# Performance work log

Hardware: AMD Instinct MI355X
Metric: run time of the kernel (lower is better)

Reference implementation:

```python
import jax, jax.numpy as jnp
import numpy as np
from jax import lax

DIM = 96
B, H, W = 4, 256, 256


def setup_inputs() -> dict:
    key = jax.random.key(0)
    ks = jax.random.split(key, 20)
    f = lambda k, s, scale=0.05: (jax.random.normal(k, s, dtype=jnp.float32) * scale)
    d = DIM
    return {
        "x": jax.random.normal(ks[0], (B, d, H, W), dtype=jnp.float32),
        "prompt": jax.random.normal(ks[1], (B, d), dtype=jnp.float32),
        "scale_weights": jax.random.uniform(ks[2], (B, 3), dtype=jnp.float32),
        "ln_w": jnp.ones((d,), jnp.float32),
        "ln_b": jnp.zeros((d,), jnp.float32),
        "e0_pw_w": f(ks[3], (d, d)),       # expert0 pointwise 1x1: [out, in]
        "e0_pw_b": f(ks[4], (d,)),
        "e0_dw_w": f(ks[5], (d, 1, 3, 3)),  # depthwise 3x3
        "e0_dw_b": f(ks[6], (d,)),
        "e1_dw_w": f(ks[7], (d, 1, 3, 3)),  # depthwise 3x3, dilation 2
        "e1_dw_b": f(ks[8], (d,)),
        "e2_dw_w": f(ks[9], (d, 1, 5, 5)),  # depthwise 5x5, dilation 3
        "e2_dw_b": f(ks[10], (d,)),
        "proj_w": f(ks[11], (d, d)),
        "proj_b": f(ks[12], (d,)),
        "ffn1_w": f(ks[13], (2 * d, d)),
        "ffn1_b": f(ks[14], (2 * d,)),
        "ffn2_w": f(ks[15], (d, 2 * d)),
        "ffn2_b": f(ks[16], (d,)),
    }


def _conv1x1(x, w, b):
    # x: [B,C,H,W], w: [O,C]
    return jnp.einsum('bchw,oc->bohw', x, w) + b[None, :, None, None]


def _dwconv(x, w, b, dilation, pad):
    # depthwise conv, w: [C,1,k,k]
    c = x.shape[1]
    y = lax.conv_general_dilated(
        x, w, window_strides=(1, 1),
        padding=[(pad, pad), (pad, pad)],
        rhs_dilation=(dilation, dilation),
        feature_group_count=c,
        dimension_numbers=('NCHW', 'OIHW', 'NCHW'))
    return y + b[None, :, None, None]


def _layernorm_c(x, w, b, eps=1e-6):
    # LayerNorm over channel dim of NCHW (torch permutes to NHWC, norms last dim)
    mu = jnp.mean(x, axis=1, keepdims=True)
    var = jnp.mean((x - mu) ** 2, axis=1, keepdims=True)
    xn = (x - mu) * lax.rsqrt(var + eps)
    return xn * w[None, :, None, None] + b[None, :, None, None]


def reference(x, prompt, scale_weights, ln_w, ln_b,
              e0_pw_w, e0_pw_b, e0_dw_w, e0_dw_b,
              e1_dw_w, e1_dw_b, e2_dw_w, e2_dw_b,
              proj_w, proj_b, ffn1_w, ffn1_b, ffn2_w, ffn2_b):
    shortcut = x
    xn = _layernorm_c(x, ln_w, ln_b)

    # Three receptive-field experts (all run densely, soft-weighted)
    e0 = _dwconv(_conv1x1(xn, e0_pw_w, e0_pw_b), e0_dw_w, e0_dw_b, dilation=1, pad=1)
    e1 = _dwconv(xn, e1_dw_w, e1_dw_b, dilation=2, pad=2)
    e2 = _dwconv(xn, e2_dw_w, e2_dw_b, dilation=3, pad=6)

    w = scale_weights  # [B,3]
    x_adaptive = (w[:, 0, None, None, None] * e0
                  + w[:, 1, None, None, None] * e1
                  + w[:, 2, None, None, None] * e2)
    x_adaptive = x_adaptive * (1.0 + prompt[:, :, None, None])

    x1 = shortcut + _conv1x1(x_adaptive, proj_w, proj_b)
    h = jax.nn.gelu(_conv1x1(x1, ffn1_w, ffn1_b), approximate=False)
    out = x1 + _conv1x1(h, ffn2_w, ffn2_b)
    return out
```

## Files before the change

### kernel.cpp

```cpp
#include <hip/hip_runtime.h>
#include <hip/hip_bf16.h>

typedef __hip_bfloat16 bf16;
typedef __attribute__((ext_vector_type(8))) __bf16 bf16x8;
typedef __attribute__((ext_vector_type(4))) float  f32x4;

#define HW   65536
#define WID  256
#define CC   96
#define NB   4
static const size_t S_ELEMS = (size_t)NB * CC * HW;

__device__ __forceinline__ float lo2f(unsigned u) { unsigned x = u << 16;        return __builtin_bit_cast(float, x); }
__device__ __forceinline__ float hi2f(unsigned u) { unsigned x = u & 0xffff0000u; return __builtin_bit_cast(float, x); }
__device__ __forceinline__ unsigned short f2bu(float f) {
    return __builtin_bit_cast(unsigned short, __float2bfloat16(f));
}

__device__ __forceinline__ float gelu_erf(float v) {
    float z  = fabsf(v) * 0.70710678118654752f;
    float t  = __builtin_amdgcn_rcpf(1.f + 0.3275911f * z);
    float poly = t * (0.254829592f + t * (-0.284496736f + t * (1.421413741f
               + t * (-1.453152027f + t * 1.061405429f))));
    float erfz = 1.f - poly * __expf(-z * z);
    float erfv = copysignf(erfz, v);
    return 0.5f * v * (1.f + erfv);
}

__global__ __launch_bounds__(256) void ln_kernel(
    const float* __restrict__ x, const float* __restrict__ lw,
    const float* __restrict__ lb, bf16* __restrict__ y)
{
    int t  = blockIdx.x * 256 + threadIdx.x;
    int b  = t >> 15;
    int hw = (t & 32767) * 2;
    size_t base = (size_t)b * CC * HW + hw;

    float s0 = 0.f, s1 = 0.f, q0 = 0.f, q1 = 0.f;
    for (int c = 0; c < CC; ++c) {
        float2 v = *reinterpret_cast<const float2*>(&x[base + (size_t)c * HW]);
        s0 += v.x; s1 += v.y; q0 += v.x * v.x; q1 += v.y * v.y;
    }
    float mu0 = s0 * (1.f / 96.f), mu1 = s1 * (1.f / 96.f);
    float rs0 = rsqrtf(q0 * (1.f / 96.f) - mu0 * mu0 + 1e-6f);
    float rs1 = rsqrtf(q1 * (1.f / 96.f) - mu1 * mu1 + 1e-6f);

    for (int c = 0; c < CC; ++c) {
        float2 v = *reinterpret_cast<const float2*>(&x[base + (size_t)c * HW]);
        float g = lw[c], be = lb[c];
        bf16 o[2];
        o[0] = __float2bfloat16((v.x - mu0) * rs0 * g + be);
        o[1] = __float2bfloat16((v.y - mu1) * rs1 * g + be);
        *reinterpret_cast<uint*>(&y[base + (size_t)c * HW]) = *reinterpret_cast<uint*>(o);
    }
}

__device__ __forceinline__ int swzo(int row, int col, int width) {
    return (row * width + col) ^ ((((row & 7) ^ ((row >> 3) & 7)) << 3));
}

template <typename TI, typename TOT, int CIN, int COUT, bool GELU, bool HASRES>
__global__ __launch_bounds__(256) void conv1x1_mfma(
    const TI* __restrict__ in, const float* __restrict__ wgt,
    const float* __restrict__ bias, const float* __restrict__ resid,
    TOT* __restrict__ out)
{
    constexpr int MT     = COUT / 16;
    constexpr int KSPLIT = CIN / 96;
    constexpr int CS     = 96;
    static_assert(CIN == KSPLIT * CS, "CIN must be 96 or 192");

    __shared__ unsigned short s_w[COUT * CIN];
    __shared__ unsigned short s_x[128 * CS];
    __shared__ float          s_b[COUT];

    const int tid  = threadIdx.x;
    const int lane = tid & 63;
    const int wave = tid >> 6;
    const int q    = lane >> 4;
    const int n    = lane & 15;

    const int pos0 = blockIdx.x * 128;
    const int b    = pos0 >> 16;
    const int hw0  = pos0 & 65535;

    constexpr int C4 = CIN / 4;
    for (int k = tid; k < COUT * C4; k += 256) {
        int o = k / C4, c4 = (k - o * C4) * 4;
        float4 w4 = *reinterpret_cast<const float4*>(&wgt[o * CIN + c4]);
        ushort4 pk = make_ushort4(f2bu(w4.x), f2bu(w4.y), f2bu(w4.z), f2bu(w4.w));
        *reinterpret_cast<ushort4*>(&s_w[swzo(o, c4, CIN)]) = pk;
    }
    for (int k = tid; k < COUT; k += 256) s_b[k] = bias[k];

    const TI* inb = in + (size_t)b * CIN * HW;

    f32x4 acc[MT][2];
#pragma unroll
    for (int mt = 0; mt < MT; ++mt) {
        acc[mt][0] = {0.f, 0.f, 0.f, 0.f};
        acc[mt][1] = {0.f, 0.f, 0.f, 0.f};
    }

    const int pl0 = wave * 32 + n;
    const int pl1 = pl0 + 16;

#pragma unroll
    for (int ks = 0; ks < KSPLIT; ++ks) {
        if (ks) __syncthreads();

        for (int idx = tid; idx < CS * 16; idx += 256) {
            const int c    = idx >> 4;
            const int pblk = idx & 15;
            const int row0 = pblk * 8;
            const TI* gp = inb + (size_t)(ks * CS + c) * HW + hw0 + row0;
            alignas(16) unsigned short u[8];
            if constexpr (__is_same(TI, float)) {
                float4 a  = *reinterpret_cast<const float4*>(gp);
                float4 b2 = *reinterpret_cast<const float4*>(gp + 4);
                u[0] = f2bu(a.x);  u[1] = f2bu(a.y);  u[2] = f2bu(a.z);  u[3] = f2bu(a.w);
                u[4] = f2bu(b2.x); u[5] = f2bu(b2.y); u[6] = f2bu(b2.z); u[7] = f2bu(b2.w);
            } else {
                *reinterpret_cast<uint4*>(u) = *reinterpret_cast<const uint4*>(gp);
            }
#pragma unroll
            for (int i = 0; i < 8; ++i)
                s_x[swzo(row0 + i, c, CS)] = u[i];
        }
        __syncthreads();

#pragma unroll
        for (int kt = 0; kt < CS / 32; ++kt) {
            const int col = kt * 32 + q * 8;
            union { unsigned short u[8]; bf16x8 v; } bf0, bf1;
            *reinterpret_cast<uint4*>(bf0.u) =
                *reinterpret_cast<const uint4*>(&s_x[swzo(pl0, col, CS)]);
            *reinterpret_cast<uint4*>(bf1.u) =
                *reinterpret_cast<const uint4*>(&s_x[swzo(pl1, col, CS)]);
#pragma unroll
            for (int mt = 0; mt < MT; ++mt) {
                union { unsigned short u[8]; bf16x8 v; } fa;
                *reinterpret_cast<uint4*>(fa.u) =
                    *reinterpret_cast<const uint4*>(&s_w[swzo(mt * 16 + n, ks * CS + col, CIN)]);
                acc[mt][0] = __builtin_amdgcn_mfma_f32_16x16x32_bf16(fa.v, bf0.v, acc[mt][0], 0, 0, 0);
                acc[mt][1] = __builtin_amdgcn_mfma_f32_16x16x32_bf16(fa.v, bf1.v, acc[mt][1], 0, 0, 0);
            }
        }
    }

    const int p0 = hw0 + pl0;
    const int p1 = hw0 + pl1;
    const size_t obase = (size_t)b * COUT * HW;
#pragma unroll
    for (int mt = 0; mt < MT; ++mt) {
#pragma unroll
        for (int nt = 0; nt < 2; ++nt) {
            const int p = (nt == 0) ? p0 : p1;
#pragma unroll
            for (int r = 0; r < 4; ++r) {
                const int o = mt * 16 + q * 4 + r;
                float v = acc[mt][nt][r] + s_b[o];
                if constexpr (GELU) v = gelu_erf(v);
                const size_t idx = obase + (size_t)o * HW + p;
                if constexpr (HASRES) v += resid[idx];
                if constexpr (__is_same(TOT, float)) out[idx] = v;
                else                                 out[idx] = __float2bfloat16(v);
            }
        }
    }
}

#define XR     20
#define XPITCH 22
#define TPITCH 10
#define XCOLS  268
#define TCOLS  258

__global__ __launch_bounds__(256) void experts_kernel(
    const bf16* __restrict__ xn, const bf16* __restrict__ t0,
    const float* __restrict__ w0, const float* __restrict__ b0,
    const float* __restrict__ w1, const float* __restrict__ b1,
    const float* __restrict__ w2, const float* __restrict__ b2,
    const float* __restrict__ sw, const float* __restrict__ prompt,
    bf16* __restrict__ xa)
{
    __shared__ alignas(16) unsigned short sxT[XCOLS * XPITCH];
    __shared__ alignas(16) unsigned short stT[TCOLS * TPITCH];

    const int tid  = threadIdx.x;
    const int lane = tid & 63;
    const int wave = tid >> 6;
    const int bid = blockIdx.x;
    const int h0  = (bid & 31) * 8;
    const int bc  = bid >> 5;
    const int b   = bc / 96;
    const int c   = bc - b * 96;
    const size_t pbase = (size_t)bc * HW;

    const bf16* xp = xn + pbase;
    const bf16* tp = t0 + pbase;
    uint* sx32 = reinterpret_cast<uint*>(sxT);
    uint* st32 = reinterpret_cast<uint*>(stT);

    if (tid < 132) {
        int cc = tid / 11, d = tid - cc * 11;
        int col = (cc < 6) ? cc : 256 + cc;
        sx32[col * 11 + d] = 0u;
    } else if (tid < 142) {
        int i = tid - 132;
        int col = (i < 5) ? 0 : 257;
        int d   = (i < 5) ? i : i - 5;
        st32[col * 5 + d] = 0u;
    }

    {
        const int rp = (lane >> 2) & 7;
        const int ch = 8 * wave + (lane & 3) + ((lane >> 5) << 2);
        const int gh0 = h0 - 6 + 2 * rp, gh1 = gh0 + 1;
        union { uint4 q; unsigned short u[8]; } a, bb;
        a.q  = ((unsigned)gh0 < 256u) ? *reinterpret_cast<const uint4*>(xp + gh0 * WID + ch * 8)
                                      : make_uint4(0u, 0u, 0u, 0u);
        bb.q = ((unsigned)gh1 < 256u) ? *reinterpret_cast<const uint4*>(xp + gh1 * WID + ch * 8)
                                      : make_uint4(0u, 0u, 0u, 0u);
        const int base = 11 * (6 + 8 * ch) + rp;
#pragma unroll
        for (int j = 0; j < 8; ++j)
            sx32[base + 11 * j] = (uint)a.u[j] | ((uint)bb.u[j] << 16);
    }
    if (wave == 2) {
        const int rp = 8 + ((lane >> 2) & 1);
        const int ch = (lane & 3) + (((lane >> 3) & 7) << 2);
        const int gh0 = h0 - 6 + 2 * rp, gh1 = gh0 + 1;
        union { uint4 q; unsigned short u[8]; } a, bb;
        a.q  = ((unsigned)gh0 < 256u) ? *reinterpret_cast<const uint4*>(xp + gh0 * WID + ch * 8)
                                      : make_uint4(0u, 0u, 0u, 0u);
        bb.q = ((unsigned)gh1 < 256u) ? *reinterpret_cast<const uint4*>(xp + gh1 * WID + ch * 8)
                                      : make_uint4(0u, 0u, 0u, 0u);
        const int base = 11 * (6 + 8 * ch) + rp;
#pragma unroll
        for (int j = 0; j < 8; ++j)
            sx32[base + 11 * j] = (uint)a.u[j] | ((uint)bb.u[j] << 16);
    }
    if (wave < 2) {
        const int rp = (lane >> 3) & 3;
        const int ch = 16 * wave + (lane & 7) + ((lane >> 5) << 3);
        const int gh0 = h0 - 1 + 2 * rp, gh1 = gh0 + 1;
        union { uint4 q; unsigned short u[8]; } a, bb;
        a.q  = ((unsigned)gh0 < 256u) ? *reinterpret_cast<const uint4*>(tp + gh0 * WID + ch * 8)
                                      : make_uint4(0u, 0u, 0u, 0u);
        bb.q = ((unsigned)gh1 < 256u) ? *reinterpret_cast<const uint4*>(tp + gh1 * WID + ch * 8)
                                      : make_uint4(0u, 0u, 0u, 0u);
        const int base = 5 * (1 + 8 * ch) + rp;
#pragma unroll
        for (int j = 0; j < 8; ++j)
            st32[base + 5 * j] = (uint)a.u[j] | ((uint)bb.u[j] << 16);
    }
    if (wave == 3 && lane < 32) {
        const int rp = 4;
        const int ch = lane;
        const int gh0 = h0 - 1 + 2 * rp, gh1 = gh0 + 1;
        union { uint4 q; unsigned short u[8]; } a, bb;
        a.q  = ((unsigned)gh0 < 256u) ? *reinterpret_cast<const uint4*>(tp + gh0 * WID + ch * 8)
                                      : make_uint4(0u, 0u, 0u, 0u);
        bb.q = ((unsigned)gh1 < 256u) ? *reinterpret_cast<const uint4*>(tp + gh1 * WID + ch * 8)
                                      : make_uint4(0u, 0u, 0u, 0u);
        const int base = 5 * (1 + 8 * ch) + rp;
#pragma unroll
        for (int j = 0; j < 8; ++j)
            st32[base + 5 * j] = (uint)a.u[j] | ((uint)bb.u[j] << 16);
    }

    float wk0[9], wk1[9], wk2[25];
#pragma unroll
    for (int i = 0; i < 9; ++i)  wk0[i] = w0[c * 9 + i];
#pragma unroll
    for (int i = 0; i < 9; ++i)  wk1[i] = w1[c * 9 + i];
#pragma unroll
    for (int i = 0; i < 25; ++i) wk2[i] = w2[c * 25 + i];
    const float bb0 = b0[c], bb1 = b1[c], bb2 = b2[c];
    const float s0 = sw[b * 3 + 0], s1 = sw[b * 3 + 1], s2 = sw[b * 3 + 2];
    const float pr = 1.f + prompt[b * 96 + c];

    __syncthreads();

    const int w = tid;
    float acc0[8], acc1[8], acc2[8];
#pragma unroll
    for (int r = 0; r < 8; ++r) { acc0[r] = bb0; acc1[r] = bb1; acc2[r] = bb2; }

    const unsigned short* bx = &sxT[w * XPITCH];
    const unsigned short* bt = &stT[w * TPITCH];

#pragma unroll
    for (int kw = 0; kw < 5; ++kw) {
        float cv[20];
#pragma unroll
        for (int j = 0; j < 10; ++j) {
            unsigned u = *reinterpret_cast<const unsigned*>(&bx[kw * 3 * XPITCH + 2 * j]);
            cv[2 * j]     = lo2f(u);
            cv[2 * j + 1] = hi2f(u);
        }
#pragma unroll
        for (int kh = 0; kh < 5; ++kh) {
            const float wv = wk2[kh * 5 + kw];
#pragma unroll
            for (int r = 0; r < 8; ++r) acc2[r] += wv * cv[r + 3 * kh];
        }
        if (kw == 2) {
#pragma unroll
            for (int kh = 0; kh < 3; ++kh) {
                const float wv = wk1[kh * 3 + 1];
#pragma unroll
                for (int r = 0; r < 8; ++r) acc1[r] += wv * cv[r + 2 * kh + 4];
            }
        }
    }
#pragma unroll
    for (int kwh = 0; kwh < 2; ++kwh) {
        const int kw = kwh * 2;
        float cv[12];
#pragma unroll
        for (int j = 0; j < 6; ++j) {
            unsigned u = *reinterpret_cast<const unsigned*>(&bx[(4 + 2 * kw) * XPITCH + 4 + 2 * j]);
            cv[2 * j]     = lo2f(u);
            cv[2 * j + 1] = hi2f(u);
        }
#pragma unroll
        for (int kh = 0; kh < 3; ++kh) {
            const float wv = wk1[kh * 3 + kw];
#pragma unroll
            for (int r = 0; r < 8; ++r) acc1[r] += wv * cv[r + 2 * kh];
        }
    }
#pragma unroll
    for (int kw = 0; kw < 3; ++kw) {
        float cv[10];
#pragma unroll
        for (int j = 0; j < 5; ++j) {
            unsigned u = *reinterpret_cast<const unsigned*>(&bt[kw * TPITCH + 2 * j]);
            cv[2 * j]     = lo2f(u);
            cv[2 * j + 1] = hi2f(u);
        }
#pragma unroll
        for (int kh = 0; kh < 3; ++kh) {
            const float wv = wk0[kh * 3 + kw];
#pragma unroll
            for (int r = 0; r < 8; ++r) acc0[r] += wv * cv[r + kh];
        }
    }

    bf16* op = xa + pbase + (size_t)h0 * WID + w;
#pragma unroll
    for (int r = 0; r < 8; ++r) {
        float v = (s0 * acc0[r] + s1 * acc1[r] + s2 * acc2[r]) * pr;
        op[r * WID] = __float2bfloat16(v);
    }
}

extern "C" void kernel_launch(void* const* d_in, const int* in_sizes, int n_in,
                              void* d_out, int out_size, void* d_ws, size_t ws_size,
                              hipStream_t stream)
{
    const float* x       = (const float*)d_in[0];
    const float* prompt  = (const float*)d_in[1];
    const float* sw      = (const float*)d_in[2];
    const float* ln_w    = (const float*)d_in[3];
    const float* ln_b    = (const float*)d_in[4];
    const float* e0_pw_w = (const float*)d_in[5];
    const float* e0_pw_b = (const float*)d_in[6];
    const float* e0_dw_w = (const float*)d_in[7];
    const float* e0_dw_b = (const float*)d_in[8];
    const float* e1_dw_w = (const float*)d_in[9];
    const float* e1_dw_b = (const float*)d_in[10];
    const float* e2_dw_w = (const float*)d_in[11];
    const float* e2_dw_b = (const float*)d_in[12];
    const float* proj_w  = (const float*)d_in[13];
    const float* proj_b  = (const float*)d_in[14];
    const float* ffn1_w  = (const float*)d_in[15];
    const float* ffn1_b  = (const float*)d_in[16];
    const float* ffn2_w  = (const float*)d_in[17];
    const float* ffn2_b  = (const float*)d_in[18];

    float* out = (float*)d_out;
    bf16*  ws  = (bf16*)d_ws;
    bf16*  A   = ws;
    bf16*  Bt  = ws + S_ELEMS;
    bf16*  Cx  = ws + 2 * S_ELEMS;
    bf16*  E   = ws;

    ln_kernel<<<512, 256, 0, stream>>>(x, ln_w, ln_b, A);
    conv1x1_mfma<bf16, bf16, 96, 96, false, false>
        <<<2048, 256, 0, stream>>>(A, e0_pw_w, e0_pw_b, nullptr, Bt);
    experts_kernel<<<12288, 256, 0, stream>>>(A, Bt, e0_dw_w, e0_dw_b, e1_dw_w, e1_dw_b,
                                              e2_dw_w, e2_dw_b, sw, prompt, Cx);
    conv1x1_mfma<bf16, float, 96, 96, false, true>
        <<<2048, 256, 0, stream>>>(Cx, proj_w, proj_b, x, out);
    conv1x1_mfma<float, bf16, 96, 192, true, false>
        <<<2048, 256, 0, stream>>>(out, ffn1_w, ffn1_b, nullptr, E);
    conv1x1_mfma<bf16, float, 192, 96, false, true>
        <<<2048, 256, 0, stream>>>(E, ffn2_w, ffn2_b, out, out);
}
```

Measured before the change: 499.0 us.

## Make conv1x1 persistent over four tiles with register-prefetched input staging

Each conv1x1 block now loops over four 128-position tiles, loading the weights into LDS once per block rather than once per tile, and the grid shrinks to 512 blocks. Input for the next K-slice or tile is prefetched into registers while the MFMAs run on the current LDS tile, then written to LDS as packed channel pairs. This targets the repeated weight conversion and the exposed global-load latency, at the cost of more registers (launch bounds now ask for 2 blocks per SM), fewer blocks in flight, and an extra barrier per tile.

```diff
diff --git a/kernel.cpp b/kernel.cpp
--- a/kernel.cpp
+++ b/kernel.cpp
@@ -59,8 +59,11 @@
     return (row * width + col) ^ ((((row & 7) ^ ((row >> 3) & 7)) << 3));
 }
 
+#define CONV_TILES 4
+#define CONV_GRID  512
+
 template <typename TI, typename TOT, int CIN, int COUT, bool GELU, bool HASRES>
-__global__ __launch_bounds__(256) void conv1x1_mfma(
+__global__ __launch_bounds__(256, 2) void conv1x1_mfma(
     const TI* __restrict__ in, const float* __restrict__ wgt,
     const float* __restrict__ bias, const float* __restrict__ resid,
     TOT* __restrict__ out)
@@ -80,10 +83,6 @@
     const int q    = lane >> 4;
     const int n    = lane & 15;
 
-    const int pos0 = blockIdx.x * 128;
-    const int b    = pos0 >> 16;
-    const int hw0  = pos0 & 65535;
-
     constexpr int C4 = CIN / 4;
     for (int k = tid; k < COUT * C4; k += 256) {
         int o = k / C4, c4 = (k - o * C4) * 4;
@@ -93,78 +92,120 @@
     }
     for (int k = tid; k < COUT; k += 256) s_b[k] = bias[k];
 
-    const TI* inb = in + (size_t)b * CIN * HW;
-
-    f32x4 acc[MT][2];
-#pragma unroll
-    for (int mt = 0; mt < MT; ++mt) {
-        acc[mt][0] = {0.f, 0.f, 0.f, 0.f};
-        acc[mt][1] = {0.f, 0.f, 0.f, 0.f};
-    }
+    uint4  pfa[3], pfb[3];
+    float4 qa0[3], qa1[3], qb0[3], qb1[3];
+
+    auto issue_pf = [&](int tg, int ks) {
+        const int pos0 = tg * 128;
+        const int bb   = pos0 >> 16;
+        const int hw0  = pos0 & 65535;
+        const TI* inb  = in + (size_t)bb * CIN * HW;
+#pragma unroll
+        for (int k = 0; k < 3; ++k) {
+            const int idx = tid + k * 256;
+            const int cp = idx >> 4, pb = idx & 15;
+            const TI* gp = inb + (size_t)(ks * CS + 2 * cp) * HW + hw0 + pb * 8;
+            if constexpr (__is_same(TI, float)) {
+                qa0[k] = *reinterpret_cast<const float4*>(gp);
+                qa1[k] = *reinterpret_cast<const float4*>(gp + 4);
+                qb0[k] = *reinterpret_cast<const float4*>(gp + HW);
+                qb1[k] = *reinterpret_cast<const float4*>(gp + HW + 4);
+            } else {
+                pfa[k] = *reinterpret_cast<const uint4*>(gp);
+                pfb[k] = *reinterpret_cast<const uint4*>(gp + HW);
+            }
+        }
+    };
+    auto write_pf = [&]() {
+#pragma unroll
+        for (int k = 0; k < 3; ++k) {
+            const int idx = tid + k * 256;
+            const int cp = idx >> 4, pb = idx & 15;
+            unsigned short ua[8], ub[8];
+            if constexpr (__is_same(TI, float)) {
+                float fa[8] = {qa0[k].x, qa0[k].y, qa0[k].z, qa0[k].w,
+                               qa1[k].x, qa1[k].y, qa1[k].z, qa1[k].w};
+                float fb[8] = {qb0[k].x, qb0[k].y, qb0[k].z, qb0[k].w,
+                               qb1[k].x, qb1[k].y, qb1[k].z, qb1[k].w};
+#pragma unroll
+                for (int i = 0; i < 8; ++i) { ua[i] = f2bu(fa[i]); ub[i] = f2bu(fb[i]); }
+            } else {
+                *reinterpret_cast<uint4*>(ua) = pfa[k];
+                *reinterpret_cast<uint4*>(ub) = pfb[k];
+            }
+#pragma unroll
+            for (int i = 0; i < 8; ++i) {
+                uint d = (uint)ua[i] | ((uint)ub[i] << 16);
+                *reinterpret_cast<uint*>(&s_x[swzo(pb * 8 + i, 2 * cp, CS)]) = d;
+            }
+        }
+    };
 
     const int pl0 = wave * 32 + n;
     const int pl1 = pl0 + 16;
 
-#pragma unroll
-    for (int ks = 0; ks < KSPLIT; ++ks) {
-        if (ks) __syncthreads();
-
-        for (int idx = tid; idx < CS * 16; idx += 256) {
-            const int c    = idx >> 4;
-            const int pblk = idx & 15;
-            const int row0 = pblk * 8;
-            const TI* gp = inb + (size_t)(ks * CS + c) * HW + hw0 + row0;
-            alignas(16) unsigned short u[8];
-            if constexpr (__is_same(TI, float)) {
-                float4 a  = *reinterpret_cast<const float4*>(gp);
-                float4 b2 = *reinterpret_cast<const float4*>(gp + 4);
-                u[0] = f2bu(a.x);  u[1] = f2bu(a.y);  u[2] = f2bu(a.z);  u[3] = f2bu(a.w);
-                u[4] = f2bu(b2.x); u[5] = f2bu(b2.y); u[6] = f2bu(b2.z); u[7] = f2bu(b2.w);
-            } else {
-                *reinterpret_cast<uint4*>(u) = *reinterpret_cast<const uint4*>(gp);
-            }
-#pragma unroll
-            for (int i = 0; i < 8; ++i)
-                s_x[swzo(row0 + i, c, CS)] = u[i];
-        }
-        __syncthreads();
-
-#pragma unroll
-        for (int kt = 0; kt < CS / 32; ++kt) {
-            const int col = kt * 32 + q * 8;
-            union { unsigned short u[8]; bf16x8 v; } bf0, bf1;
-            *reinterpret_cast<uint4*>(bf0.u) =
-                *reinterpret_cast<const uint4*>(&s_x[swzo(pl0, col, CS)]);
-            *reinterpret_cast<uint4*>(bf1.u) =
-                *reinterpret_cast<const uint4*>(&s_x[swzo(pl1, col, CS)]);
-#pragma unroll
-            for (int mt = 0; mt < MT; ++mt) {
-                union { unsigned short u[8]; bf16x8 v; } fa;
-                *reinterpret_cast<uint4*>(fa.u) =
-                    *reinterpret_cast<const uint4*>(&s_w[swzo(mt * 16 + n, ks * CS + col, CIN)]);
-                acc[mt][0] = __builtin_amdgcn_mfma_f32_16x16x32_bf16(fa.v, bf0.v, acc[mt][0], 0, 0, 0);
-                acc[mt][1] = __builtin_amdgcn_mfma_f32_16x16x32_bf16(fa.v, bf1.v, acc[mt][1], 0, 0, 0);
-            }
-        }
-    }
-
-    const int p0 = hw0 + pl0;
-    const int p1 = hw0 + pl1;
-    const size_t obase = (size_t)b * COUT * HW;
-#pragma unroll
-    for (int mt = 0; mt < MT; ++mt) {
-#pragma unroll
-        for (int nt = 0; nt < 2; ++nt) {
-            const int p = (nt == 0) ? p0 : p1;
-#pragma unroll
-            for (int r = 0; r < 4; ++r) {
-                const int o = mt * 16 + q * 4 + r;
-                float v = acc[mt][nt][r] + s_b[o];
-                if constexpr (GELU) v = gelu_erf(v);
-                const size_t idx = obase + (size_t)o * HW + p;
-                if constexpr (HASRES) v += resid[idx];
-                if constexpr (__is_same(TOT, float)) out[idx] = v;
-                else                                 out[idx] = __float2bfloat16(v);
+    issue_pf(blockIdx.x * CONV_TILES, 0);
+    __syncthreads();
+
+    for (int t = 0; t < CONV_TILES; ++t) {
+        const int tg   = blockIdx.x * CONV_TILES + t;
+        const int pos0 = tg * 128;
+        const int b    = pos0 >> 16;
+        const int hw0  = pos0 & 65535;
+
+        f32x4 acc[MT][2];
+#pragma unroll
+        for (int mt = 0; mt < MT; ++mt) {
+            acc[mt][0] = {0.f, 0.f, 0.f, 0.f};
+            acc[mt][1] = {0.f, 0.f, 0.f, 0.f};
+        }
+
+#pragma unroll
+        for (int ks = 0; ks < KSPLIT; ++ks) {
+            write_pf();
+            __syncthreads();
+            if (ks + 1 < KSPLIT)            issue_pf(tg, ks + 1);
+            else if (t + 1 < CONV_TILES)    issue_pf(tg + 1, 0);
+
+#pragma unroll
+            for (int kt = 0; kt < CS / 32; ++kt) {
+                const int col = kt * 32 + q * 8;
+                union { unsigned short u[8]; bf16x8 v; } bf0, bf1;
+                *reinterpret_cast<uint4*>(bf0.u) =
+                    *reinterpret_cast<const uint4*>(&s_x[swzo(pl0, col, CS)]);
+                *reinterpret_cast<uint4*>(bf1.u) =
+                    *reinterpret_cast<const uint4*>(&s_x[swzo(pl1, col, CS)]);
+#pragma unroll
+                for (int mt = 0; mt < MT; ++mt) {
+                    union { unsigned short u[8]; bf16x8 v; } fa;
+                    *reinterpret_cast<uint4*>(fa.u) =
+                        *reinterpret_cast<const uint4*>(&s_w[swzo(mt * 16 + n, ks * CS + col, CIN)]);
+                    acc[mt][0] = __builtin_amdgcn_mfma_f32_16x16x32_bf16(fa.v, bf0.v, acc[mt][0], 0, 0, 0);
+                    acc[mt][1] = __builtin_amdgcn_mfma_f32_16x16x32_bf16(fa.v, bf1.v, acc[mt][1], 0, 0, 0);
+                }
+            }
+            if (ks + 1 < KSPLIT || t + 1 < CONV_TILES)
+                __syncthreads();
+        }
+
+        const int p0 = hw0 + pl0;
+        const int p1 = hw0 + pl1;
+        const size_t obase = (size_t)b * COUT * HW;
+#pragma unroll
+        for (int mt = 0; mt < MT; ++mt) {
+#pragma unroll
+            for (int nt = 0; nt < 2; ++nt) {
+                const int p = (nt == 0) ? p0 : p1;
+#pragma unroll
+                for (int r = 0; r < 4; ++r) {
+                    const int o = mt * 16 + q * 4 + r;
+                    float v = acc[mt][nt][r] + s_b[o];
+                    if constexpr (GELU) v = gelu_erf(v);
+                    const size_t idx = obase + (size_t)o * HW + p;
+                    if constexpr (HASRES) v += resid[idx];
+                    if constexpr (__is_same(TOT, float)) out[idx] = v;
+                    else                                 out[idx] = __float2bfloat16(v);
+                }
             }
         }
     }
@@ -390,13 +431,13 @@
 
     ln_kernel<<<512, 256, 0, stream>>>(x, ln_w, ln_b, A);
     conv1x1_mfma<bf16, bf16, 96, 96, false, false>
-        <<<2048, 256, 0, stream>>>(A, e0_pw_w, e0_pw_b, nullptr, Bt);
+        <<<CONV_GRID, 256, 0, stream>>>(A, e0_pw_w, e0_pw_b, nullptr, Bt);
     experts_kernel<<<12288, 256, 0, stream>>>(A, Bt, e0_dw_w, e0_dw_b, e1_dw_w, e1_dw_b,
                                               e2_dw_w, e2_dw_b, sw, prompt, Cx);
     conv1x1_mfma<bf16, float, 96, 96, false, true>
-        <<<2048, 256, 0, stream>>>(Cx, proj_w, proj_b, x, out);
+        <<<CONV_GRID, 256, 0, stream>>>(Cx, proj_w, proj_b, x, out);
     conv1x1_mfma<float, bf16, 96, 192, true, false>
-        <<<2048, 256, 0, stream>>>(out, ffn1_w, ffn1_b, nullptr, E);
+        <<<CONV_GRID, 256, 0, stream>>>(out, ffn1_w, ffn1_b, nullptr, E);
     conv1x1_mfma<bf16, float, 192, 96, false, true>
-        <<<2048, 256, 0, stream>>>(E, ffn2_w, ffn2_b, out, out);
-}
+        <<<CONV_GRID, 256, 0, stream>>>(E, ffn2_w, ffn2_b, out, out);
+}
```

Measured after the change: 600.8 us. 20.4% more time.

## Split 1x1 conv output channels into 96-wide chunks to shrink LDS and registers

Applied to the files above, without the earlier changes.

Restructures the MFMA 1x1 conv kernel so output channels are processed in 96-channel slices, with only a 96x96 weight tile staged in shared memory per slice and accumulators sized for 6 M-tiles. This cuts LDS use (notably for the 192-wide FFN weights) and accumulator registers, aiming for higher occupancy. The input staging also now packs two channels per 32-bit LDS store, halving the number of shared-memory writes. In exchange, weights are reloaded and converted per slice, and for CIN=192 the input tile is reloaded once per output slice, which adds global traffic and extra barriers.

```diff
diff --git a/kernel.cpp b/kernel.cpp
--- a/kernel.cpp
+++ b/kernel.cpp
@@ -65,13 +65,13 @@
     const float* __restrict__ bias, const float* __restrict__ resid,
     TOT* __restrict__ out)
 {
-    constexpr int MT     = COUT / 16;
     constexpr int KSPLIT = CIN / 96;
-    constexpr int CS     = 96;
-    static_assert(CIN == KSPLIT * CS, "CIN must be 96 or 192");
-
-    __shared__ unsigned short s_w[COUT * CIN];
-    __shared__ unsigned short s_x[128 * CS];
+    constexpr int OSPLIT = COUT / 96;
+    constexpr int MT     = 6;
+    static_assert(CIN == KSPLIT * 96 && COUT == OSPLIT * 96, "96-multiples only");
+
+    __shared__ unsigned short s_w[96 * 96];
+    __shared__ unsigned short s_x[128 * 96];
     __shared__ float          s_b[COUT];
 
     const int tid  = threadIdx.x;
@@ -84,87 +84,97 @@
     const int b    = pos0 >> 16;
     const int hw0  = pos0 & 65535;
 
-    constexpr int C4 = CIN / 4;
-    for (int k = tid; k < COUT * C4; k += 256) {
-        int o = k / C4, c4 = (k - o * C4) * 4;
-        float4 w4 = *reinterpret_cast<const float4*>(&wgt[o * CIN + c4]);
-        ushort4 pk = make_ushort4(f2bu(w4.x), f2bu(w4.y), f2bu(w4.z), f2bu(w4.w));
-        *reinterpret_cast<ushort4*>(&s_w[swzo(o, c4, CIN)]) = pk;
-    }
     for (int k = tid; k < COUT; k += 256) s_b[k] = bias[k];
 
     const TI* inb = in + (size_t)b * CIN * HW;
-
-    f32x4 acc[MT][2];
-#pragma unroll
-    for (int mt = 0; mt < MT; ++mt) {
-        acc[mt][0] = {0.f, 0.f, 0.f, 0.f};
-        acc[mt][1] = {0.f, 0.f, 0.f, 0.f};
-    }
-
     const int pl0 = wave * 32 + n;
     const int pl1 = pl0 + 16;
 
 #pragma unroll
-    for (int ks = 0; ks < KSPLIT; ++ks) {
-        if (ks) __syncthreads();
-
-        for (int idx = tid; idx < CS * 16; idx += 256) {
-            const int c    = idx >> 4;
-            const int pblk = idx & 15;
-            const int row0 = pblk * 8;
-            const TI* gp = inb + (size_t)(ks * CS + c) * HW + hw0 + row0;
-            alignas(16) unsigned short u[8];
-            if constexpr (__is_same(TI, float)) {
-                float4 a  = *reinterpret_cast<const float4*>(gp);
-                float4 b2 = *reinterpret_cast<const float4*>(gp + 4);
-                u[0] = f2bu(a.x);  u[1] = f2bu(a.y);  u[2] = f2bu(a.z);  u[3] = f2bu(a.w);
-                u[4] = f2bu(b2.x); u[5] = f2bu(b2.y); u[6] = f2bu(b2.z); u[7] = f2bu(b2.w);
-            } else {
-                *reinterpret_cast<uint4*>(u) = *reinterpret_cast<const uint4*>(gp);
+    for (int os = 0; os < OSPLIT; ++os) {
+        f32x4 acc[MT][2];
+#pragma unroll
+        for (int mt = 0; mt < MT; ++mt) {
+            acc[mt][0] = {0.f, 0.f, 0.f, 0.f};
+            acc[mt][1] = {0.f, 0.f, 0.f, 0.f};
+        }
+
+#pragma unroll
+        for (int ks = 0; ks < KSPLIT; ++ks) {
+            for (int k = tid; k < 96 * 24; k += 256) {
+                int o = k / 24, c4 = (k - o * 24) * 4;
+                float4 w4 = *reinterpret_cast<const float4*>(
+                    &wgt[(size_t)(os * 96 + o) * CIN + ks * 96 + c4]);
+                ushort4 pk = make_ushort4(f2bu(w4.x), f2bu(w4.y), f2bu(w4.z), f2bu(w4.w));
+                *reinterpret_cast<ushort4*>(&s_w[swzo(o, c4, 96)]) = pk;
             }
-#pragma unroll
-            for (int i = 0; i < 8; ++i)
-                s_x[swzo(row0 + i, c, CS)] = u[i];
-        }
-        __syncthreads();
-
-#pragma unroll
-        for (int kt = 0; kt < CS / 32; ++kt) {
-            const int col = kt * 32 + q * 8;
-            union { unsigned short u[8]; bf16x8 v; } bf0, bf1;
-            *reinterpret_cast<uint4*>(bf0.u) =
-                *reinterpret_cast<const uint4*>(&s_x[swzo(pl0, col, CS)]);
-            *reinterpret_cast<uint4*>(bf1.u) =
-                *reinterpret_cast<const uint4*>(&s_x[swzo(pl1, col, CS)]);
-#pragma unroll
-            for (int mt = 0; mt < MT; ++mt) {
-                union { unsigned short u[8]; bf16x8 v; } fa;
-                *reinterpret_cast<uint4*>(fa.u) =
-                    *reinterpret_cast<const uint4*>(&s_w[swzo(mt * 16 + n, ks * CS + col, CIN)]);
-                acc[mt][0] = __builtin_amdgcn_mfma_f32_16x16x32_bf16(fa.v, bf0.v, acc[mt][0], 0, 0, 0);
-                acc[mt][1] = __builtin_amdgcn_mfma_f32_16x16x32_bf16(fa.v, bf1.v, acc[mt][1], 0, 0, 0);
+            if (KSPLIT > 1 || os == 0) {
+                for (int idx = tid; idx < 48 * 16; idx += 256) {
+                    const int cp = idx >> 4;
+                    const int pb = idx & 15;
+                    const TI* gp = inb + (size_t)(ks * 96 + 2 * cp) * HW + hw0 + pb * 8;
+                    unsigned short ua[8], ub[8];
+                    if constexpr (__is_same(TI, float)) {
+                        float4 a0 = *reinterpret_cast<const float4*>(gp);
+                        float4 a1 = *reinterpret_cast<const float4*>(gp + 4);
+                        float4 b0 = *reinterpret_cast<const float4*>(gp + HW);
+                        float4 b1 = *reinterpret_cast<const float4*>(gp + HW + 4);
+                        ua[0]=f2bu(a0.x); ua[1]=f2bu(a0.y); ua[2]=f2bu(a0.z); ua[3]=f2bu(a0.w);
+                        ua[4]=f2bu(a1.x); ua[5]=f2bu(a1.y); ua[6]=f2bu(a1.z); ua[7]=f2bu(a1.w);
+                        ub[0]=f2bu(b0.x); ub[1]=f2bu(b0.y); ub[2]=f2bu(b0.z); ub[3]=f2bu(b0.w);
+                        ub[4]=f2bu(b1.x); ub[5]=f2bu(b1.y); ub[6]=f2bu(b1.z); ub[7]=f2bu(b1.w);
+                    } else {
+                        *reinterpret_cast<uint4*>(ua) = *reinterpret_cast<const uint4*>(gp);
+                        *reinterpret_cast<uint4*>(ub) = *reinterpret_cast<const uint4*>(gp + HW);
+                    }
+#pragma unroll
+                    for (int i = 0; i < 8; ++i) {
+                        uint d = (uint)ua[i] | ((uint)ub[i] << 16);
+                        *reinterpret_cast<uint*>(&s_x[swzo(pb * 8 + i, 2 * cp, 96)]) = d;
+                    }
+                }
             }
-        }
-    }
-
-    const int p0 = hw0 + pl0;
-    const int p1 = hw0 + pl1;
-    const size_t obase = (size_t)b * COUT * HW;
-#pragma unroll
-    for (int mt = 0; mt < MT; ++mt) {
-#pragma unroll
-        for (int nt = 0; nt < 2; ++nt) {
-            const int p = (nt == 0) ? p0 : p1;
-#pragma unroll
-            for (int r = 0; r < 4; ++r) {
-                const int o = mt * 16 + q * 4 + r;
-                float v = acc[mt][nt][r] + s_b[o];
-                if constexpr (GELU) v = gelu_erf(v);
-                const size_t idx = obase + (size_t)o * HW + p;
-                if constexpr (HASRES) v += resid[idx];
-                if constexpr (__is_same(TOT, float)) out[idx] = v;
-                else                                 out[idx] = __float2bfloat16(v);
+            __syncthreads();
+
+#pragma unroll
+            for (int kt = 0; kt < 3; ++kt) {
+                const int col = kt * 32 + q * 8;
+                union { unsigned short u[8]; bf16x8 v; } bf0, bf1;
+                *reinterpret_cast<uint4*>(bf0.u) =
+                    *reinterpret_cast<const uint4*>(&s_x[swzo(pl0, col, 96)]);
+                *reinterpret_cast<uint4*>(bf1.u) =
+                    *reinterpret_cast<const uint4*>(&s_x[swzo(pl1, col, 96)]);
+#pragma unroll
+                for (int mt = 0; mt < MT; ++mt) {
+                    union { unsigned short u[8]; bf16x8 v; } fa;
+                    *reinterpret_cast<uint4*>(fa.u) =
+                        *reinterpret_cast<const uint4*>(&s_w[swzo(mt * 16 + n, col, 96)]);
+                    acc[mt][0] = __builtin_amdgcn_mfma_f32_16x16x32_bf16(fa.v, bf0.v, acc[mt][0], 0, 0, 0);
+                    acc[mt][1] = __builtin_amdgcn_mfma_f32_16x16x32_bf16(fa.v, bf1.v, acc[mt][1], 0, 0, 0);
+                }
+            }
+            if (os + 1 < OSPLIT || ks + 1 < KSPLIT)
+                __syncthreads();
+        }
+
+        const int p0 = hw0 + pl0;
+        const int p1 = hw0 + pl1;
+        const size_t obase = (size_t)b * COUT * HW;
+#pragma unroll
+        for (int mt = 0; mt < MT; ++mt) {
+#pragma unroll
+            for (int nt = 0; nt < 2; ++nt) {
+                const int p = (nt == 0) ? p0 : p1;
+#pragma unroll
+                for (int r = 0; r < 4; ++r) {
+                    const int o = os * 96 + mt * 16 + q * 4 + r;
+                    float v = acc[mt][nt][r] + s_b[o];
+                    if constexpr (GELU) v = gelu_erf(v);
+                    const size_t idx = obase + (size_t)o * HW + p;
+                    if constexpr (HASRES) v += resid[idx];
+                    if constexpr (__is_same(TOT, float)) out[idx] = v;
+                    else                                 out[idx] = __float2bfloat16(v);
+                }
             }
         }
     }
```

Result: faster. 484.7 us (-2.9%).
